# Kernel tuning notes

Hardware: AMD Instinct MI355X
Metric: run time of the kernel (lower is better)

Reference implementation:

```python
import jax, jax.numpy as jnp
import numpy as np

B = 8            # number of point clouds in the batch
NT = 8192        # target points per cloud
NS = 2048        # source points per cloud
K = 3            # knn_interpolate neighbors
C_TGT = 128      # target (skip) feature channels
C_SRC = 256      # source feature channels
C_IN = C_TGT + C_SRC   # 384 = mlp_channels[0]
C_HID = 256            # mlp_channels[1]
C_OUT = 128            # mlp_channels[2]
EPS = 1e-16


def setup_inputs() -> dict:
    key = jax.random.key(0)
    ks = jax.random.split(key, 10)
    Nt, Ns = B * NT, B * NS
    s1 = 1.0 / np.sqrt(C_IN)
    s2 = 1.0 / np.sqrt(C_HID)
    return {
        "x_target": jax.random.normal(ks[0], (Nt, C_TGT), jnp.float32),
        "pos_target": jax.random.normal(ks[1], (Nt, 3), jnp.float32),
        "batch_target": (jnp.arange(Nt, dtype=jnp.int32) // NT).astype(jnp.int32),
        "x_source": jax.random.normal(ks[2], (Ns, C_SRC), jnp.float32),
        "pos_source": jax.random.normal(ks[3], (Ns, 3), jnp.float32),
        "batch_source": (jnp.arange(Ns, dtype=jnp.int32) // NS).astype(jnp.int32),
        "W1": jax.random.normal(ks[4], (C_IN, C_HID), jnp.float32) * s1,
        "b1": jnp.zeros((C_HID,), jnp.float32),
        "W2": jax.random.normal(ks[5], (C_HID, C_OUT), jnp.float32) * s2,
        "b2": jnp.zeros((C_OUT,), jnp.float32),
        "Ws": jax.random.normal(ks[6], (C_IN, C_OUT), jnp.float32) * s1,
        "bs": jnp.zeros((C_OUT,), jnp.float32),
    }


def _knn_interpolate(x_source, pos_source, pos_target):
    """PyG knn_interpolate with inverse-squared-distance weights.
    Batches are contiguous equal-size blocks -> reshape to [B, N, ...]."""
    pt = pos_target.reshape(B, NT, 3)
    ps = pos_source.reshape(B, NS, 3)
    xs = x_source.reshape(B, NS, C_SRC)
    # squared pairwise distances [B, NT, NS]
    d2 = jnp.sum((pt[:, :, None, :] - ps[:, None, :, :]) ** 2, axis=-1)
    neg, idx = jax.lax.top_k(-d2, K)            # idx: [B, NT, K]
    w = 1.0 / jnp.clip(-neg, EPS)               # inverse squared distance
    gathered = jax.vmap(lambda x, i: x[i])(xs, idx)  # [B, NT, K, C_SRC]
    interp = jnp.sum(w[..., None] * gathered, axis=2) / jnp.sum(w, axis=2)[..., None]
    return interp.reshape(B * NT, C_SRC)


def reference(x_target, pos_target, batch_target, x_source, pos_source,
              batch_source, W1, b1, W2, b2, Ws, bs):
    interpolated = _knn_interpolate(x_source, pos_source, pos_target)
    combined = jnp.concatenate([x_target, interpolated], axis=1)  # [Nt, 384]
    h = jax.nn.relu(combined @ W1 + b1) @ W2 + b2                 # MLP branch
    res = combined @ Ws + bs                                      # shortcut
    return jax.nn.relu(h + res)
```

## Files before the change

### kernel.cpp

```cpp
#include <hip/hip_runtime.h>
#include <hip/hip_bf16.h>

#define B_    8
#define NT_   8192
#define NS_   2048
#define NTOT  (B_ * NT_)
#define CTGT  128
#define CSRC  256
#define CIN   384
#define CHID  256
#define COUT  128

typedef __bf16 bf16x8 __attribute__((ext_vector_type(8)));
typedef float  f32x4  __attribute__((ext_vector_type(4)));
typedef unsigned short u16x8 __attribute__((ext_vector_type(8)));

__device__ inline unsigned short f2bf(float f) {
    unsigned int u = __float_as_uint(f);
    u += 0x7FFF + ((u >> 16) & 1);
    return (unsigned short)(u >> 16);
}

__device__ __forceinline__ void gload16(const unsigned short* g, unsigned short* l) {
    __builtin_amdgcn_global_load_lds(
        (const __attribute__((address_space(1))) unsigned int*)g,
        (__attribute__((address_space(3))) unsigned int*)l, 16, 0, 0);
}

__device__ __forceinline__ void stage_ab(
    const unsigned short* __restrict__ ga, int ldA,
    const unsigned short* __restrict__ gb, int ldB,
    unsigned short* Alds, unsigned short* Blds,
    int k0, int widu, int lane) {
    int rloc = lane >> 2;
    int cswz = ((lane & 3) ^ ((lane >> 3) & 3)) * 8;
#pragma unroll
    for (int i = 0; i < 2; ++i) {
        int c = widu * 2 + i;
        int row = c * 16 + rloc;
        gload16(ga + (size_t)row * ldA + k0 + cswz, Alds + c * 512);
        gload16(gb + (size_t)row * ldB + k0 + cswz, Blds + c * 512);
    }
}

__global__ __launch_bounds__(256) void prep_weights(
    const float* __restrict__ W1, const float* __restrict__ Ws,
    const float* __restrict__ W2,
    unsigned short* __restrict__ Wct, unsigned short* __restrict__ W2t) {
    int g = blockIdx.x * 256 + threadIdx.x;
    if (g < CIN * CIN) {
        int n = g / CIN, k = g % CIN;
        float v = (n < CHID) ? W1[(size_t)k * CHID + n]
                             : Ws[(size_t)k * COUT + (n - CHID)];
        Wct[g] = f2bf(v);
    } else {
        int g2 = g - CIN * CIN;
        if (g2 < COUT * CHID) {
            int n = g2 / CHID, k = g2 % CHID;
            W2t[g2] = f2bf(W2[(size_t)k * COUT + n]);
        }
    }
}

__global__ __launch_bounds__(256) void knn_kernel(
    const float* __restrict__ pos_t, const float* __restrict__ pos_s,
    int* __restrict__ knn_i, float* __restrict__ knn_d) {
    __shared__ char smem[32768];
    float4* ps4 = (float4*)smem;
    float*  md  = (float*)smem;
    int*    mi  = (int*)(smem + 6144);

    int blk = blockIdx.x;
    int batch = blk >> 7;
    const float* src = pos_s + (size_t)batch * NS_ * 3;
    for (int i = threadIdx.x; i < NS_; i += 256) {
        ps4[i] = make_float4(src[i * 3 + 0], src[i * 3 + 1], src[i * 3 + 2], 0.0f);
    }
    __syncthreads();

    int tl = threadIdx.x & 31;
    int ck = threadIdx.x >> 5;
    int tA = blk * 64 + tl;
    int tB = tA + 32;
    float ax = pos_t[tA * 3 + 0], ay = pos_t[tA * 3 + 1], az = pos_t[tA * 3 + 2];
    float bx = pos_t[tB * 3 + 0], by = pos_t[tB * 3 + 1], bz = pos_t[tB * 3 + 2];

    float a0 = 3.4e38f, a1 = 3.4e38f, a2 = 3.4e38f;
    float b0 = 3.4e38f, b1 = 3.4e38f, b2 = 3.4e38f;
    int ia0 = 0, ia1 = 0, ia2 = 0, ib0 = 0, ib1 = 0, ib2 = 0;
    int jbeg = ck * 256, jend = jbeg + 256;
#pragma unroll 2
    for (int j = jbeg; j < jend; ++j) {
        float4 p = ps4[j];
        float dax = __fsub_rn(ax, p.x);
        float day = __fsub_rn(ay, p.y);
        float daz = __fsub_rn(az, p.z);
        float da = __fadd_rn(__fadd_rn(__fmul_rn(dax, dax), __fmul_rn(day, day)),
                             __fmul_rn(daz, daz));
        float dbx = __fsub_rn(bx, p.x);
        float dby = __fsub_rn(by, p.y);
        float dbz = __fsub_rn(bz, p.z);
        float db = __fadd_rn(__fadd_rn(__fmul_rn(dbx, dbx), __fmul_rn(dby, dby)),
                             __fmul_rn(dbz, dbz));
        if (da < a2) {
            if (da < a1) {
                a2 = a1; ia2 = ia1;
                if (da < a0) { a1 = a0; ia1 = ia0; a0 = da; ia0 = j; }
                else         { a1 = da; ia1 = j; }
            } else { a2 = da; ia2 = j; }
        }
        if (db < b2) {
            if (db < b1) {
                b2 = b1; ib2 = ib1;
                if (db < b0) { b1 = b0; ib1 = ib0; b0 = db; ib0 = j; }
                else         { b1 = db; ib1 = j; }
            } else { b2 = db; ib2 = j; }
        }
    }
    __syncthreads();

    int sA = (tl * 8 + ck) * 3;
    int sB = ((tl + 32) * 8 + ck) * 3;
    md[sA + 0] = a0; md[sA + 1] = a1; md[sA + 2] = a2;
    mi[sA + 0] = ia0; mi[sA + 1] = ia1; mi[sA + 2] = ia2;
    md[sB + 0] = b0; md[sB + 1] = b1; md[sB + 2] = b2;
    mi[sB + 0] = ib0; mi[sB + 1] = ib1; mi[sB + 2] = ib2;
    __syncthreads();

    if (threadIdx.x < 64) {
        int tloc = threadIdx.x;
        int t = blk * 64 + tloc;
        int base = tloc * 24;
        float e0 = md[base + 0], e1 = md[base + 1], e2 = md[base + 2];
        int   j0 = mi[base + 0], j1 = mi[base + 1], j2 = mi[base + 2];
#pragma unroll
        for (int c = 1; c < 8; ++c) {
#pragma unroll
            for (int r = 0; r < 3; ++r) {
                float d = md[base + c * 3 + r];
                int   i = mi[base + c * 3 + r];
                if (d < e2) {
                    if (d < e1) {
                        e2 = e1; j2 = j1;
                        if (d < e0) { e1 = e0; j1 = j0; e0 = d; j0 = i; }
                        else        { e1 = d;  j1 = i; }
                    } else { e2 = d; j2 = i; }
                }
            }
        }
        knn_i[t * 3 + 0] = j0; knn_i[t * 3 + 1] = j1; knn_i[t * 3 + 2] = j2;
        knn_d[t * 3 + 0] = e0; knn_d[t * 3 + 1] = e1; knn_d[t * 3 + 2] = e2;
    }
}

__global__ __launch_bounds__(256) void interp_kernel(
    const float* __restrict__ x_t, const float* __restrict__ x_s,
    const int* __restrict__ knn_i, const float* __restrict__ knn_d,
    unsigned short* __restrict__ combined) {
    int g = blockIdx.x * 256 + threadIdx.x;
    int row = g / 96, seg = g % 96;
    if (row >= NTOT) return;
    if (seg < 32) {
        float4 v = *(const float4*)(x_t + (size_t)row * CTGT + seg * 4);
        ushort4 o;
        o.x = f2bf(v.x); o.y = f2bf(v.y); o.z = f2bf(v.z); o.w = f2bf(v.w);
        *(ushort4*)(combined + (size_t)row * CIN + seg * 4) = o;
    } else {
        int c = (seg - 32) * 4;
        int batch = row >> 13;
        const float* xsb = x_s + (size_t)batch * NS_ * CSRC;
        int i0 = knn_i[row * 3 + 0];
        int i1 = knn_i[row * 3 + 1];
        int i2 = knn_i[row * 3 + 2];
        float w0 = 1.0f / fmaxf(knn_d[row * 3 + 0], 1e-16f);
        float w1 = 1.0f / fmaxf(knn_d[row * 3 + 1], 1e-16f);
        float w2 = 1.0f / fmaxf(knn_d[row * 3 + 2], 1e-16f);
        float inv = 1.0f / (w0 + w1 + w2);
        float4 a = *(const float4*)(xsb + (size_t)i0 * CSRC + c);
        float4 b = *(const float4*)(xsb + (size_t)i1 * CSRC + c);
        float4 d = *(const float4*)(xsb + (size_t)i2 * CSRC + c);
        ushort4 o;
        o.x = f2bf((w0 * a.x + w1 * b.x + w2 * d.x) * inv);
        o.y = f2bf((w0 * a.y + w1 * b.y + w2 * d.y) * inv);
        o.z = f2bf((w0 * a.z + w1 * b.z + w2 * d.z) * inv);
        o.w = f2bf((w0 * a.w + w1 * b.w + w2 * d.w) * inv);
        *(ushort4*)(combined + (size_t)row * CIN + CTGT + c) = o;
    }
}

__global__ __launch_bounds__(256) void gemm1_kernel(
    const unsigned short* __restrict__ A, const unsigned short* __restrict__ Bt,
    const float* __restrict__ b1, const float* __restrict__ bs,
    unsigned short* __restrict__ hbuf, float* __restrict__ resbuf) {
    __shared__ unsigned short Alds[2][128 * 32];
    __shared__ unsigned short Blds[2][128 * 32];
    int tid = threadIdx.x;
    int wid = tid >> 6, lane = tid & 63;
    int widu = __builtin_amdgcn_readfirstlane(wid);
    int wm = wid >> 1, wn = wid & 1;
    int r = lane & 15, g = lane >> 4;
    int kcol = (g * 8) ^ (((r >> 1) & 3) * 8);

    const unsigned short* ga = A  + (size_t)(blockIdx.x * 128) * CIN;
    const unsigned short* gb = Bt + (size_t)(blockIdx.y * 128) * CIN;

    f32x4 acc[4][4] = {};

    stage_ab(ga, CIN, gb, CIN, Alds[0], Blds[0], 0, widu, lane);
    __syncthreads();
    int cur = 0;
#pragma unroll 1
    for (int t = 0; t < 12; ++t) {
        if (t + 1 < 12)
            stage_ab(ga, CIN, gb, CIN, Alds[cur ^ 1], Blds[cur ^ 1],
                     (t + 1) * 32, widu, lane);
        bf16x8 af[4], bf[4];
#pragma unroll
        for (int mi = 0; mi < 4; ++mi)
            af[mi] = *(const bf16x8*)(&Alds[cur][(wm * 64 + mi * 16 + r) * 32 + kcol]);
#pragma unroll
        for (int ni = 0; ni < 4; ++ni)
            bf[ni] = *(const bf16x8*)(&Blds[cur][(wn * 64 + ni * 16 + r) * 32 + kcol]);
#pragma unroll
        for (int mi = 0; mi < 4; ++mi)
#pragma unroll
            for (int ni = 0; ni < 4; ++ni)
                acc[mi][ni] = __builtin_amdgcn_mfma_f32_16x16x32_bf16(
                    af[mi], bf[ni], acc[mi][ni], 0, 0, 0);
        __syncthreads();
        cur ^= 1;
    }

    int r0 = g * 4;
#pragma unroll
    for (int mi = 0; mi < 4; ++mi)
#pragma unroll
        for (int ni = 0; ni < 4; ++ni) {
            int n = blockIdx.y * 128 + wn * 64 + ni * 16 + r;
#pragma unroll
            for (int rr = 0; rr < 4; ++rr) {
                int m = blockIdx.x * 128 + wm * 64 + mi * 16 + r0 + rr;
                float v = acc[mi][ni][rr];
                if (n < CHID) {
                    v += b1[n];
                    v = fmaxf(v, 0.0f);
                    hbuf[(size_t)m * CHID + n] = f2bf(v);
                } else {
                    int n2 = n - CHID;
                    resbuf[(size_t)m * COUT + n2] = v + bs[n2];
                }
            }
        }
}

__global__ __launch_bounds__(256) void gemm2_kernel(
    const unsigned short* __restrict__ A, const unsigned short* __restrict__ Bt,
    const float* __restrict__ b2, const float* __restrict__ resbuf,
    float* __restrict__ out) {
    __shared__ unsigned short Alds[2][128 * 32];
    __shared__ unsigned short Blds[2][128 * 32];
    int tid = threadIdx.x;
    int wid = tid >> 6, lane = tid & 63;
    int widu = __builtin_amdgcn_readfirstlane(wid);
    int wm = wid >> 1, wn = wid & 1;
    int r = lane & 15, g = lane >> 4;
    int kcol = (g * 8) ^ (((r >> 1) & 3) * 8);

    const unsigned short* ga = A + (size_t)(blockIdx.x * 128) * CHID;

    f32x4 acc[4][4] = {};

    stage_ab(ga, CHID, Bt, CHID, Alds[0], Blds[0], 0, widu, lane);
    __syncthreads();
    int cur = 0;
#pragma unroll 1
    for (int t = 0; t < 8; ++t) {
        if (t + 1 < 8)
            stage_ab(ga, CHID, Bt, CHID, Alds[cur ^ 1], Blds[cur ^ 1],
                     (t + 1) * 32, widu, lane);
        bf16x8 af[4], bf[4];
#pragma unroll
        for (int mi = 0; mi < 4; ++mi)
            af[mi] = *(const bf16x8*)(&Alds[cur][(wm * 64 + mi * 16 + r) * 32 + kcol]);
#pragma unroll
        for (int ni = 0; ni < 4; ++ni)
            bf[ni] = *(const bf16x8*)(&Blds[cur][(wn * 64 + ni * 16 + r) * 32 + kcol]);
#pragma unroll
        for (int mi = 0; mi < 4; ++mi)
#pragma unroll
            for (int ni = 0; ni < 4; ++ni)
                acc[mi][ni] = __builtin_amdgcn_mfma_f32_16x16x32_bf16(
                    af[mi], bf[ni], acc[mi][ni], 0, 0, 0);
        __syncthreads();
        cur ^= 1;
    }

    int r0 = g * 4;
#pragma unroll
    for (int mi = 0; mi < 4; ++mi)
#pragma unroll
        for (int ni = 0; ni < 4; ++ni) {
            int n = wn * 64 + ni * 16 + r;
#pragma unroll
            for (int rr = 0; rr < 4; ++rr) {
                int m = blockIdx.x * 128 + wm * 64 + mi * 16 + r0 + rr;
                float v = acc[mi][ni][rr] + b2[n] + resbuf[(size_t)m * COUT + n];
                out[(size_t)m * COUT + n] = fmaxf(v, 0.0f);
            }
        }
}

extern "C" void kernel_launch(void* const* d_in, const int* in_sizes, int n_in,
                              void* d_out, int out_size, void* d_ws, size_t ws_size,
                              hipStream_t stream) {
    const float* x_t   = (const float*)d_in[0];
    const float* pos_t = (const float*)d_in[1];
    const float* x_s   = (const float*)d_in[3];
    const float* pos_s = (const float*)d_in[4];
    const float* W1    = (const float*)d_in[6];
    const float* b1    = (const float*)d_in[7];
    const float* W2    = (const float*)d_in[8];
    const float* b2    = (const float*)d_in[9];
    const float* Ws    = (const float*)d_in[10];
    const float* bs    = (const float*)d_in[11];

    char* ws = (char*)d_ws;
    int*            knn_i  = (int*)           (ws + 0);
    float*          knn_d  = (float*)         (ws + 786432);
    unsigned short* Wct    = (unsigned short*)(ws + 1572864);
    unsigned short* W2t    = (unsigned short*)(ws + 1867776);
    unsigned short* comb   = (unsigned short*)(ws + 1933312);
    unsigned short* hbuf   = (unsigned short*)(ws + 52264960);
    float*          resbuf = (float*)         (ws + 85819392);
    float*          out    = (float*)d_out;

    prep_weights<<<704, 256, 0, stream>>>(W1, Ws, W2, Wct, W2t);
    knn_kernel<<<NTOT / 64, 256, 0, stream>>>(pos_t, pos_s, knn_i, knn_d);
    interp_kernel<<<(NTOT * 96) / 256, 256, 0, stream>>>(x_t, x_s, knn_i, knn_d, comb);
    dim3 g1(NTOT / 128, CIN / 128);
    gemm1_kernel<<<g1, 256, 0, stream>>>(comb, Wct, b1, bs, hbuf, resbuf);
    gemm2_kernel<<<NTOT / 128, 256, 0, stream>>>(hbuf, W2t, b2, resbuf, out);
}
```

Measured before the change: 271.7 us.

## Use branchless med3 top-3 insertion in KNN and remap gemm1 block order

The KNN top-3 insertion, in both the scan loop and the merge step, is rewritten as a branchless form built on fmed3/fmin and selects, and the scan loop's unroll factor goes from 2 to 4. This targets divergent branching in the inner distance loop. The GEMM1 grid becomes a 1D launch whose block IDs are remapped so the three N-tiles of one M-row run together and consecutive IDs are spread across XCD groups, aiming at better L2 reuse of the A tile. The branchless form executes every instruction on every iteration, whereas before most lanes skipped the update.

```diff
diff --git a/kernel.cpp b/kernel.cpp
--- a/kernel.cpp
+++ b/kernel.cpp
@@ -89,7 +89,7 @@
     float b0 = 3.4e38f, b1 = 3.4e38f, b2 = 3.4e38f;
     int ia0 = 0, ia1 = 0, ia2 = 0, ib0 = 0, ib1 = 0, ib2 = 0;
     int jbeg = ck * 256, jend = jbeg + 256;
-#pragma unroll 2
+#pragma unroll 4
     for (int j = jbeg; j < jend; ++j) {
         float4 p = ps4[j];
         float dax = __fsub_rn(ax, p.x);
@@ -102,19 +102,27 @@
         float dbz = __fsub_rn(bz, p.z);
         float db = __fadd_rn(__fadd_rn(__fmul_rn(dbx, dbx), __fmul_rn(dby, dby)),
                              __fmul_rn(dbz, dbz));
-        if (da < a2) {
-            if (da < a1) {
-                a2 = a1; ia2 = ia1;
-                if (da < a0) { a1 = a0; ia1 = ia0; a0 = da; ia0 = j; }
-                else         { a1 = da; ia1 = j; }
-            } else { a2 = da; ia2 = j; }
-        }
-        if (db < b2) {
-            if (db < b1) {
-                b2 = b1; ib2 = ib1;
-                if (db < b0) { b1 = b0; ib1 = ib0; b0 = db; ib0 = j; }
-                else         { b1 = db; ib1 = j; }
-            } else { b2 = db; ib2 = j; }
+        {
+            bool c0 = da < a0, c1 = da < a1, c2 = da < a2;
+            int ni2 = c2 ? (c1 ? ia1 : j) : ia2;
+            int ni1 = c1 ? (c0 ? ia0 : j) : ia1;
+            int ni0 = c0 ? j : ia0;
+            float na2 = __builtin_amdgcn_fmed3f(da, a1, a2);
+            float na1 = __builtin_amdgcn_fmed3f(da, a0, a1);
+            float na0 = fminf(a0, da);
+            a0 = na0; a1 = na1; a2 = na2;
+            ia0 = ni0; ia1 = ni1; ia2 = ni2;
+        }
+        {
+            bool c0 = db < b0, c1 = db < b1, c2 = db < b2;
+            int ni2 = c2 ? (c1 ? ib1 : j) : ib2;
+            int ni1 = c1 ? (c0 ? ib0 : j) : ib1;
+            int ni0 = c0 ? j : ib0;
+            float nb2 = __builtin_amdgcn_fmed3f(db, b1, b2);
+            float nb1 = __builtin_amdgcn_fmed3f(db, b0, b1);
+            float nb0 = fminf(b0, db);
+            b0 = nb0; b1 = nb1; b2 = nb2;
+            ib0 = ni0; ib1 = ni1; ib2 = ni2;
         }
     }
     __syncthreads();
@@ -139,13 +147,15 @@
             for (int r = 0; r < 3; ++r) {
                 float d = md[base + c * 3 + r];
                 int   i = mi[base + c * 3 + r];
-                if (d < e2) {
-                    if (d < e1) {
-                        e2 = e1; j2 = j1;
-                        if (d < e0) { e1 = e0; j1 = j0; e0 = d; j0 = i; }
-                        else        { e1 = d;  j1 = i; }
-                    } else { e2 = d; j2 = i; }
-                }
+                bool c0 = d < e0, c1 = d < e1, c2 = d < e2;
+                int nj2 = c2 ? (c1 ? j1 : i) : j2;
+                int nj1 = c1 ? (c0 ? j0 : i) : j1;
+                int nj0 = c0 ? i : j0;
+                float ne2 = __builtin_amdgcn_fmed3f(d, e1, e2);
+                float ne1 = __builtin_amdgcn_fmed3f(d, e0, e1);
+                float ne0 = fminf(e0, d);
+                e0 = ne0; e1 = ne1; e2 = ne2;
+                j0 = nj0; j1 = nj1; j2 = nj2;
             }
         }
         knn_i[t * 3 + 0] = j0; knn_i[t * 3 + 1] = j1; knn_i[t * 3 + 2] = j2;
@@ -194,6 +204,9 @@
     unsigned short* __restrict__ hbuf, float* __restrict__ resbuf) {
     __shared__ unsigned short Alds[2][128 * 32];
     __shared__ unsigned short Blds[2][128 * 32];
+    int id = blockIdx.x;
+    int sid = (id & 7) * 192 + (id >> 3);
+    int bm = sid / 3, bn = sid - bm * 3;
     int tid = threadIdx.x;
     int wid = tid >> 6, lane = tid & 63;
     int widu = __builtin_amdgcn_readfirstlane(wid);
@@ -201,8 +214,8 @@
     int r = lane & 15, g = lane >> 4;
     int kcol = (g * 8) ^ (((r >> 1) & 3) * 8);
 
-    const unsigned short* ga = A  + (size_t)(blockIdx.x * 128) * CIN;
-    const unsigned short* gb = Bt + (size_t)(blockIdx.y * 128) * CIN;
+    const unsigned short* ga = A  + (size_t)(bm * 128) * CIN;
+    const unsigned short* gb = Bt + (size_t)(bn * 128) * CIN;
 
     f32x4 acc[4][4] = {};
 
@@ -236,10 +249,10 @@
     for (int mi = 0; mi < 4; ++mi)
 #pragma unroll
         for (int ni = 0; ni < 4; ++ni) {
-            int n = blockIdx.y * 128 + wn * 64 + ni * 16 + r;
+            int n = bn * 128 + wn * 64 + ni * 16 + r;
 #pragma unroll
             for (int rr = 0; rr < 4; ++rr) {
-                int m = blockIdx.x * 128 + wm * 64 + mi * 16 + r0 + rr;
+                int m = bm * 128 + wm * 64 + mi * 16 + r0 + rr;
                 float v = acc[mi][ni][rr];
                 if (n < CHID) {
                     v += b1[n];
@@ -337,7 +350,6 @@
     prep_weights<<<704, 256, 0, stream>>>(W1, Ws, W2, Wct, W2t);
     knn_kernel<<<NTOT / 64, 256, 0, stream>>>(pos_t, pos_s, knn_i, knn_d);
     interp_kernel<<<(NTOT * 96) / 256, 256, 0, stream>>>(x_t, x_s, knn_i, knn_d, comb);
-    dim3 g1(NTOT / 128, CIN / 128);
-    gemm1_kernel<<<g1, 256, 0, stream>>>(comb, Wct, b1, bs, hbuf, resbuf);
+    gemm1_kernel<<<1536, 256, 0, stream>>>(comb, Wct, b1, bs, hbuf, resbuf);
     gemm2_kernel<<<NTOT / 128, 256, 0, stream>>>(hbuf, W2t, b2, resbuf, out);
 }
```

Measured after the change: 261.9 us. 3.6% less time.
